# Kernel tuning notes

Measured on AMD Instinct MI355X. Metric: run time of the kernel, lower is better.

The kernel has to match this reference:

```python
import jax, jax.numpy as jnp
import numpy as np

H = 50  # hidden_size
IN = 3  # input_size
OUT = 7


def _lstm_layer(x, Wih, Whh, bih, bhh):
    # x: [B, T, D]; Wih: [4H, D]; Whh: [4H, H]; biases: [4H]
    # Precompute input-side gate pre-activations once (torch adds both biases).
    xg = jnp.einsum('btd,gd->btg', x, Wih) + bih + bhh  # [B, T, 4H]
    B = x.shape[0]
    h0 = jnp.zeros((B, H), x.dtype)
    c0 = jnp.zeros((B, H), x.dtype)

    def step(carry, xt):
        h, c = carry
        gates = xt + h @ Whh.T  # [B, 4H]
        i, f, g, o = jnp.split(gates, 4, axis=-1)  # torch gate order: i,f,g,o
        i = jax.nn.sigmoid(i)
        f = jax.nn.sigmoid(f)
        g = jnp.tanh(g)
        o = jax.nn.sigmoid(o)
        c = f * c + i * g
        h = o * jnp.tanh(c)
        return (h, c), h

    (_, _), hs = jax.lax.scan(step, (h0, c0), jnp.swapaxes(xg, 0, 1))  # hs: [T, B, H]
    return jnp.swapaxes(hs, 0, 1)  # [B, T, H]


def setup_inputs() -> dict:
    key = jax.random.key(0)
    ks = jax.random.split(key, 11)
    s = 1.0 / np.sqrt(H)  # torch LSTM init scale
    B, T = 4096, 512
    return {
        'x': jax.random.normal(ks[0], (B, T, IN), jnp.float32),
        'Wih0': jax.random.uniform(ks[1], (4 * H, IN), jnp.float32, -s, s),
        'Whh0': jax.random.uniform(ks[2], (4 * H, H), jnp.float32, -s, s),
        'bih0': jax.random.uniform(ks[3], (4 * H,), jnp.float32, -s, s),
        'bhh0': jax.random.uniform(ks[4], (4 * H,), jnp.float32, -s, s),
        'Wih1': jax.random.uniform(ks[5], (4 * H, H), jnp.float32, -s, s),
        'Whh1': jax.random.uniform(ks[6], (4 * H, H), jnp.float32, -s, s),
        'bih1': jax.random.uniform(ks[7], (4 * H,), jnp.float32, -s, s),
        'bhh1': jax.random.uniform(ks[8], (4 * H,), jnp.float32, -s, s),
        'Wfc': jax.random.uniform(ks[9], (OUT, H), jnp.float32, -s, s),
        'bfc': jax.random.uniform(ks[10], (OUT,), jnp.float32, -s, s),
    }


def reference(x, Wih0, Whh0, bih0, bhh0, Wih1, Whh1, bih1, bhh1, Wfc, bfc):
    h1 = _lstm_layer(x, Wih0, Whh0, bih0, bhh0)   # [B, T, H]
    h2 = _lstm_layer(h1, Wih1, Whh1, bih1, bhh1)  # [B, T, H]
    last = h2[:, -1, :]                           # [B, H]
    return last @ Wfc.T + bfc                     # [B, 7]
```

## Files before the change

kernel.cpp:

```cpp
#include <hip/hip_runtime.h>

#define HD 50
#define TT 512
#define BRR 16
#define TC 32
#define KS 136

using f16   = _Float16;
using f16x8 = __attribute__((ext_vector_type(8))) f16;
using f32x4 = __attribute__((ext_vector_type(4))) float;

#define LOG2E 1.4426950408889634f

__device__ __forceinline__ short f2h_bits(float f) {
    f16 h = (f16)f;
    return *reinterpret_cast<short*>(&h);
}
__device__ __forceinline__ float h2f(short b) {
    f16 h = *reinterpret_cast<f16*>(&b);
    return (float)h;
}
__device__ __forceinline__ float frcp(float x) { return __builtin_amdgcn_rcpf(x); }
#if __has_builtin(__builtin_amdgcn_exp2f)
__device__ __forceinline__ float fexp2(float x) { return __builtin_amdgcn_exp2f(x); }
#else
__device__ __forceinline__ float fexp2(float x) { return exp2f(x); }
#endif

__global__ __launch_bounds__(512, 2) void lstm2_uni2(
    const float* __restrict__ x,
    const float* __restrict__ Wih0, const float* __restrict__ Whh0,
    const float* __restrict__ bih0, const float* __restrict__ bhh0,
    const float* __restrict__ Wih1, const float* __restrict__ Whh1,
    const float* __restrict__ bih1, const float* __restrict__ bhh1,
    const float* __restrict__ Wfc, const float* __restrict__ bfc,
    float* __restrict__ out)
{
    __shared__ short s_A[2][BRR][KS];
    __shared__ float s_xs[2][BRR][TC * 3];

    const int tid  = threadIdx.x;
    const int wid  = tid >> 6;
    const int lane = tid & 63;
    const int lr   = lane & 15;
    const int lq   = lane >> 4;
    const int r0   = blockIdx.x * BRR;

    const int  p     = 8 * lr + wid;
    const bool valid = (p < 100);
    const bool isL1  = valid && (p >= 50);
    const int  u     = valid ? (isL1 ? p - 50 : p) : 0;
    const int  wcol  = isL1 ? 64 + u : u;

    f16x8 bw[4][4];
    float bvT[4];
    #pragma unroll
    for (int tt = 0; tt < 4; ++tt) {
        const float sc = (tt == 2) ? (2.0f * LOG2E) : (-LOG2E);
        const int g = tt * HD + u;
        if (!isL1) {
            bvT[tt] = valid ? (bih0[g] + bhh0[g]) * sc : 0.f;
            #pragma unroll
            for (int s = 0; s < 4; ++s) {
                #pragma unroll
                for (int j = 0; j < 8; ++j) {
                    const int k = s*32 + lq*8 + j;
                    float wv = 0.f;
                    if (valid) {
                        if (k < HD) wv = Whh0[g*HD + k];
                        else if (k < HD + 3) wv = Wih0[g*3 + (k - HD)];
                    }
                    bw[tt][s][j] = (f16)(wv * sc);
                }
            }
        } else {
            bvT[tt] = (bih1[g] + bhh1[g]) * sc;
            #pragma unroll
            for (int s = 0; s < 4; ++s) {
                #pragma unroll
                for (int j = 0; j < 8; ++j) {
                    const int k = s*32 + lq*8 + j;
                    float wv = 0.f;
                    if (k < HD) wv = Wih1[g*HD + k];
                    else if (k >= 64 && k < 64 + HD) wv = Whh1[g*HD + (k - 64)];
                    bw[tt][s][j] = (f16)(wv * sc);
                }
            }
        }
    }

    float cst[4] = {0.f, 0.f, 0.f, 0.f};

    const bool xduty = (wid < 4) && (lr >= 13);
    const int  xidx  = wid * 12 + (lr - 13) * 4 + lq;
    const int  xrow  = xidx / 3, xd = xidx % 3;

    for (int q = tid; q < 2 * BRR * KS; q += 512) ((short*)s_A)[q] = 0;
    for (int q = tid; q < BRR * TC * 3; q += 512) {
        const int rr = q / (TC * 3), qq = q % (TC * 3);
        s_xs[0][rr][qq] = x[(size_t)(r0 + rr) * (TT * 3) + qq];
    }
    __syncthreads();
    if (xduty) s_A[0][xrow][HD + xd] = f2h_bits(s_xs[0][xrow][xd]);
    __syncthreads();

    for (int n = 0; n <= TT; ++n) {
        const char* ab = (const char*)&s_A[n & 1][0][0];
        f16x8 a[4];
        #pragma unroll
        for (int s = 0; s < 4; ++s)
            a[s] = *(const f16x8*)(ab + lr * (2 * KS) + s * 64 + lq * 16);
        f32x4 acc[4];
        #pragma unroll
        for (int tt = 0; tt < 4; ++tt) { const float b = bvT[tt]; acc[tt] = (f32x4){b, b, b, b}; }
        #pragma unroll
        for (int s = 0; s < 4; ++s) {
            #pragma unroll
            for (int tt = 0; tt < 4; ++tt)
                acc[tt] = __builtin_amdgcn_mfma_f32_16x16x32_f16(a[s], bw[tt][s], acc[tt], 0, 0, 0);
        }

        const bool act = valid && (isL1 ? (n >= 1) : (n < TT));
        if (act) {
            #pragma unroll
            for (int j = 0; j < 4; ++j) {
                const float ei = fexp2(acc[0][j]);
                const float ef = fexp2(acc[1][j]);
                const float eg = fexp2(acc[2][j]);
                const float eo = fexp2(acc[3][j]);
                const float ig = (eg - 1.0f) * frcp((eg + 1.0f) * (1.0f + ei));
                const float fv = frcp(1.0f + ef);
                const float c  = fv * cst[j] + ig;
                cst[j] = c;
                const float ec = fexp2(c * (2.0f * LOG2E));
                const float h  = (ec - 1.0f) * frcp((ec + 1.0f) * (1.0f + eo));
                s_A[(n + 1) & 1][lq * 4 + j][wcol] = f2h_bits(h);
            }
        }
        if (xduty && (n + 1) < TT) {
            const int tn = n + 1;
            s_A[(n + 1) & 1][xrow][HD + xd] =
                f2h_bits(s_xs[(tn / TC) & 1][xrow][(tn % TC) * 3 + xd]);
        }
        {
            const int t2s = n + 2;
            if (t2s < TT && (t2s % TC) == 0) {
                const int cb = (t2s / TC) & 1;
                for (int q = tid; q < BRR * TC * 3; q += 512) {
                    const int rr = q / (TC * 3), qq = q % (TC * 3);
                    s_xs[cb][rr][qq] = x[(size_t)(r0 + rr) * (TT * 3) + (size_t)t2s * 3 + qq];
                }
            }
        }
        __syncthreads();
    }

    if (tid < BRR * 7) {
        const int r = tid / 7, o = tid % 7;
        float acc = bfc[o];
        #pragma unroll
        for (int uu = 0; uu < HD; ++uu)
            acc += h2f(s_A[1][r][64 + uu]) * Wfc[o * HD + uu];
        out[(size_t)(r0 + r) * 7 + o] = acc;
    }
}

extern "C" void kernel_launch(void* const* d_in, const int* in_sizes, int n_in,
                              void* d_out, int out_size, void* d_ws, size_t ws_size,
                              hipStream_t stream) {
    const float* xp    = (const float*)d_in[0];
    const float* Wih0  = (const float*)d_in[1];
    const float* Whh0  = (const float*)d_in[2];
    const float* bih0  = (const float*)d_in[3];
    const float* bhh0  = (const float*)d_in[4];
    const float* Wih1  = (const float*)d_in[5];
    const float* Whh1  = (const float*)d_in[6];
    const float* bih1  = (const float*)d_in[7];
    const float* bhh1  = (const float*)d_in[8];
    const float* Wfc   = (const float*)d_in[9];
    const float* bfc   = (const float*)d_in[10];
    float* outp = (float*)d_out;

    const int B = in_sizes[0] / (TT * 3);
    const int grid = B / BRR;

    lstm2_uni2<<<grid, 512, 0, stream>>>(
        xp, Wih0, Whh0, bih0, bhh0, Wih1, Whh1, bih1, bhh1, Wfc, bfc, outp);
}
```

Before: 399.1 us.

## Split MFMA accumulator chains and pack gate math into paired reciprocals

```diff
diff --git a/kernel.cpp b/kernel.cpp
--- a/kernel.cpp
+++ b/kernel.cpp
@@ -9,6 +9,7 @@
 using f16   = _Float16;
 using f16x8 = __attribute__((ext_vector_type(8))) f16;
 using f32x4 = __attribute__((ext_vector_type(4))) float;
+using f32x2 = __attribute__((ext_vector_type(2))) float;
 
 #define LOG2E 1.4426950408889634f
 
@@ -27,7 +28,7 @@
 __device__ __forceinline__ float fexp2(float x) { return exp2f(x); }
 #endif
 
-__global__ __launch_bounds__(512, 2) void lstm2_uni2(
+__global__ __launch_bounds__(512, 2) void lstm2_pk(
     const float* __restrict__ x,
     const float* __restrict__ Wih0, const float* __restrict__ Whh0,
     const float* __restrict__ bih0, const float* __restrict__ bhh0,
@@ -89,7 +90,7 @@
         }
     }
 
-    float cst[4] = {0.f, 0.f, 0.f, 0.f};
+    f32x2 cstp[2] = { (f32x2){0.f, 0.f}, (f32x2){0.f, 0.f} };
 
     const bool xduty = (wid < 4) && (lr >= 13);
     const int  xidx  = wid * 12 + (lr - 13) * 4 + lq;
@@ -104,38 +105,68 @@
     if (xduty) s_A[0][xrow][HD + xd] = f2h_bits(s_xs[0][xrow][xd]);
     __syncthreads();
 
+    #pragma unroll 2
     for (int n = 0; n <= TT; ++n) {
         const char* ab = (const char*)&s_A[n & 1][0][0];
         f16x8 a[4];
         #pragma unroll
         for (int s = 0; s < 4; ++s)
             a[s] = *(const f16x8*)(ab + lr * (2 * KS) + s * 64 + lq * 16);
+        f32x4 accE[4], accO[4];
+        #pragma unroll
+        for (int tt = 0; tt < 4; ++tt) {
+            const float b = bvT[tt];
+            accE[tt] = (f32x4){b, b, b, b};
+            accO[tt] = (f32x4){0.f, 0.f, 0.f, 0.f};
+        }
+        #pragma unroll
+        for (int s = 0; s < 4; ++s) {
+            if ((s & 1) == 0) {
+                #pragma unroll
+                for (int tt = 0; tt < 4; ++tt)
+                    accE[tt] = __builtin_amdgcn_mfma_f32_16x16x32_f16(a[s], bw[tt][s], accE[tt], 0, 0, 0);
+            } else {
+                #pragma unroll
+                for (int tt = 0; tt < 4; ++tt)
+                    accO[tt] = __builtin_amdgcn_mfma_f32_16x16x32_f16(a[s], bw[tt][s], accO[tt], 0, 0, 0);
+            }
+        }
         f32x4 acc[4];
         #pragma unroll
-        for (int tt = 0; tt < 4; ++tt) { const float b = bvT[tt]; acc[tt] = (f32x4){b, b, b, b}; }
-        #pragma unroll
-        for (int s = 0; s < 4; ++s) {
-            #pragma unroll
-            for (int tt = 0; tt < 4; ++tt)
-                acc[tt] = __builtin_amdgcn_mfma_f32_16x16x32_f16(a[s], bw[tt][s], acc[tt], 0, 0, 0);
-        }
+        for (int tt = 0; tt < 4; ++tt) acc[tt] = accE[tt] + accO[tt];
 
         const bool act = valid && (isL1 ? (n >= 1) : (n < TT));
         if (act) {
+            f32x2 hv2[2];
             #pragma unroll
-            for (int j = 0; j < 4; ++j) {
-                const float ei = fexp2(acc[0][j]);
-                const float ef = fexp2(acc[1][j]);
-                const float eg = fexp2(acc[2][j]);
-                const float eo = fexp2(acc[3][j]);
-                const float ig = (eg - 1.0f) * frcp((eg + 1.0f) * (1.0f + ei));
-                const float fv = frcp(1.0f + ef);
-                const float c  = fv * cst[j] + ig;
-                cst[j] = c;
-                const float ec = fexp2(c * (2.0f * LOG2E));
-                const float h  = (ec - 1.0f) * frcp((ec + 1.0f) * (1.0f + eo));
-                s_A[(n + 1) & 1][lq * 4 + j][wcol] = f2h_bits(h);
-            }
+            for (int hp = 0; hp < 2; ++hp) {
+                const int j0 = 2 * hp, j1 = 2 * hp + 1;
+                const f32x2 ei = { fexp2(acc[0][j0]), fexp2(acc[0][j1]) };
+                const f32x2 ef = { fexp2(acc[1][j0]), fexp2(acc[1][j1]) };
+                const f32x2 eg = { fexp2(acc[2][j0]), fexp2(acc[2][j1]) };
+                const f32x2 eo = { fexp2(acc[3][j0]), fexp2(acc[3][j1]) };
+                const f32x2 D1 = (eg + 1.0f) * (ei + 1.0f);
+                const f32x2 D2 = ef + 1.0f;
+                const f32x2 P  = D1 * D2;
+                const f32x2 num1 = eg - 1.0f;
+                const float r1 = frcp(P.x * P.y);
+                const f32x2 iP = r1 * __builtin_shufflevector(P, P, 1, 0);
+                const f32x2 ig = num1 * (iP * D2);
+                const f32x2 fv = iP * D1;
+                const f32x2 c  = fv * cstp[hp] + ig;
+                cstp[hp] = c;
+                const f32x2 ecarg = c * (2.0f * LOG2E);
+                const f32x2 ec = { fexp2(ecarg.x), fexp2(ecarg.y) };
+                const f32x2 num2 = ec - 1.0f;
+                const f32x2 den2 = (ec + 1.0f) * (eo + 1.0f);
+                const float r2 = frcp(den2.x * den2.y);
+                const f32x2 iD = r2 * __builtin_shufflevector(den2, den2, 1, 0);
+                hv2[hp] = num2 * iD;
+            }
+            s_A[(n + 1) & 1][lq * 4 + 0][wcol] = f2h_bits(hv2[0].x);
+            s_A[(n + 1) & 1][lq * 4 + 1][wcol] = f2h_bits(hv2[0].y);
+            s_A[(n + 1) & 1][lq * 4 + 2][wcol] = f2h_bits(hv2[1].x);
+            s_A[(n + 1) & 1][lq * 4 + 3][wcol] = f2h_bits(hv2[1].y);
         }
         if (xduty && (n + 1) < TT) {
             const int tn = n + 1;
@@ -184,6 +215,6 @@
     const int B = in_sizes[0] / (TT * 3);
     const int grid = B / BRR;
 
-    lstm2_uni2<<<grid, 512, 0, stream>>>(
+    lstm2_pk<<<grid, 512, 0, stream>>>(
         xp, Wih0, Whh0, bih0, bhh0, Wih1, Whh1, bih1, bhh1, Wfc, bfc, outp);
 }
```

Result: faster. 376.9 us (-5.6%).
